# Optimization experiments

Measured on AMD Instinct MI355X. Metric: run time of the kernel, lower is better.

Reference implementation:

```python
import jax, jax.numpy as jnp
import numpy as np

B, S, D = 4, 2048, 2048
H, HD = 16, 128
ROPE_THETA = 10000.0


def rotate_half(x):
    half = x.shape[-1] // 2
    return jnp.concatenate([-x[..., half:], x[..., :half]], axis=-1)


def setup_inputs() -> dict:
    key = jax.random.key(0)
    ks = jax.random.split(key, 5)
    scale = 1.0 / np.sqrt(D)
    x = jax.random.normal(ks[0], (B, S, D), dtype=jnp.float32)
    wq = jax.random.normal(ks[1], (D, H * HD), dtype=jnp.float32) * scale
    wk = jax.random.normal(ks[2], (D, H * HD), dtype=jnp.float32) * scale
    wv = jax.random.normal(ks[3], (D, H * HD), dtype=jnp.float32) * scale
    wo = jax.random.normal(ks[4], (H * HD, D), dtype=jnp.float32) * scale
    # RoPE frequencies: freqs_cis real/imag parts, shape [S, HD//2]
    inv_freq = 1.0 / (ROPE_THETA ** (np.arange(0, HD, 2, dtype=np.float32) / HD))
    t = np.arange(S, dtype=np.float32)
    freqs = np.outer(t, inv_freq)  # [S, HD//2]
    cos = jnp.asarray(np.cos(freqs), dtype=jnp.float32)
    sin = jnp.asarray(np.sin(freqs), dtype=jnp.float32)
    return {"x": x, "wq": wq, "wk": wk, "wv": wv, "wo": wo, "cos": cos, "sin": sin}


def reference(x, wq, wk, wv, wo, cos, sin):
    batch, seq_len, _ = x.shape
    # QKV projections (no bias), reshape to [b, h, s, d]
    q = (x @ wq).reshape(batch, seq_len, H, HD).transpose(0, 2, 1, 3)
    k = (x @ wk).reshape(batch, seq_len, H, HD).transpose(0, 2, 1, 3)
    v = (x @ wv).reshape(batch, seq_len, H, HD)  # [b, s, h, d]
    # RoPE (half-split / rotate_half convention)
    cos_full = jnp.concatenate([cos, cos], axis=-1)[None, None, :seq_len, :]
    sin_full = jnp.concatenate([sin, sin], axis=-1)[None, None, :seq_len, :]
    q = q * cos_full + rotate_half(q) * sin_full
    k = k * cos_full + rotate_half(k) * sin_full
    # Scaled dot-product attention with causal mask
    logits = jnp.einsum('bhqd,bhkd->bhqk', q, k) / jnp.sqrt(jnp.float32(HD))
    causal = jnp.tril(jnp.ones((seq_len, seq_len), dtype=bool))
    logits = jnp.where(causal[None, None, :, :], logits, -1e10)
    weights = jax.nn.softmax(logits, axis=-1)
    out = jnp.einsum('bhqk,bkhd->bqhd', weights, v)
    out = out.reshape(batch, seq_len, H * HD)
    return out @ wo
```

## Files before the change

### kernel.cpp

```cpp
#include <hip/hip_runtime.h>
#include <cstdint>
#include <cstddef>

typedef unsigned short u16;
using bf16x8  = __attribute__((ext_vector_type(8))) short;
using floatx4 = __attribute__((ext_vector_type(4))) float;

__device__ __forceinline__ u16 f2bf(float f) {
    union { float f; unsigned u; } v; v.f = f;
    unsigned r = v.u + 0x7fffu + ((v.u >> 16) & 1u);
    return (u16)(r >> 16);
}
__device__ __forceinline__ float bf2f(u16 h) {
    union { unsigned u; float f; } v; v.u = ((unsigned)h) << 16; return v.f;
}
__device__ __forceinline__ floatx4 mfma16(bf16x8 a, bf16x8 b, floatx4 c) {
    return __builtin_amdgcn_mfma_f32_16x16x32_bf16(a, b, c, 0, 0, 0);
}
using gptr_t = const __attribute__((address_space(1))) unsigned int*;
using lptr_t = __attribute__((address_space(3))) unsigned int*;
__device__ __forceinline__ void lds16(const void* g, void* l) {
    __builtin_amdgcn_global_load_lds((gptr_t)g, (lptr_t)l, 16, 0, 0);
}
typedef __attribute__((address_space(3))) const u16* lds_cp;
__device__ __forceinline__ bf16x8 dsr128(const u16* p) {
    bf16x8 r;
    asm volatile("ds_read_b128 %0, %1" : "=v"(r) : "v"((lds_cp)p));
    return r;
}

#define ATT_SCALE 0.1275758218522532f

__global__ __launch_bounds__(256) void cvt_x(const float* __restrict__ x, u16* __restrict__ xb) {
    size_t i = ((size_t)blockIdx.x * 256 + threadIdx.x) * 4;
    float4 v = *(const float4*)&x[i];
    ushort4 r; r.x = f2bf(v.x); r.y = f2bf(v.y); r.z = f2bf(v.z); r.w = f2bf(v.w);
    *(ushort4*)&xb[i] = r;
}

__global__ __launch_bounds__(256) void transpose_wall(const float* __restrict__ wq, const float* __restrict__ wk,
                                                      const float* __restrict__ wv, const float* __restrict__ wo,
                                                      u16* __restrict__ wqkvb, u16* __restrict__ wob) {
    __shared__ float t[64][65];
    const int z = blockIdx.z;
    const float* in = (z == 0) ? wq : (z == 1) ? wk : (z == 2) ? wv : wo;
    u16* out = (z < 3) ? (wqkvb + (size_t)z * 2048 * 2048) : wob;
    int k0 = blockIdx.x * 64, n0 = blockIdx.y * 64;
    int tx = threadIdx.x, ty = threadIdx.y;
#pragma unroll
    for (int i = 0; i < 16; ++i) {
        int r = i * 4 + ty;
        t[r][tx] = in[(size_t)(k0 + r) * 2048 + n0 + tx];
    }
    __syncthreads();
#pragma unroll
    for (int i = 0; i < 16; ++i) {
        int r = i * 4 + ty;
        out[(size_t)(n0 + r) * 2048 + k0 + tx] = f2bf(t[tx][r]);
    }
}

template <int MODE>
__global__ __launch_bounds__(512, 2) void gemm_bt(const u16* __restrict__ A, const u16* __restrict__ B,
                                                  u16* __restrict__ Qo, u16* __restrict__ Ko, u16* __restrict__ Vt,
                                                  float* __restrict__ Co) {
    __shared__ __align__(16) u16 sA[2][16384];
    __shared__ __align__(16) u16 sB[2][16384];

    const int nbx = (MODE == 0) ? 24 : 8;
    const int bid = blockIdx.x;
    const int q8 = (int)gridDim.x >> 3;
    const int wg = (bid & 7) * q8 + (bid >> 3);
    const int bx = wg % nbx, by = wg / nbx;
    const int m0 = by << 8, n0 = bx << 8;

    const int tid = threadIdx.x;
    const int w = tid >> 6, lane = tid & 63;
    const int wm = w >> 2, wn = w & 3;
    const int m16 = lane & 15, q4 = lane >> 4;
    const int lr = lane >> 3;
    const int lc8 = (lane & 7) ^ lr;

    const u16* Ag = A + (size_t)(m0 + w * 16 + lr) * 2048 + lc8 * 8;
    const u16* Bg = B + (size_t)(n0 + w * 16 + lr) * 2048 + lc8 * 8;

    const int swz0 = ((q4 ^ (m16 & 7)) << 3);
    const int swz1 = (((4 + q4) ^ (m16 & 7)) << 3);

    floatx4 acc[8][4];
#pragma unroll
    for (int r = 0; r < 8; ++r)
#pragma unroll
        for (int c = 0; c < 4; ++c) acc[r][c] = (floatx4)0.0f;
    bf16x8 af[4][2];
    bf16x8 bf[4][2];

#define STAGE_A(b, h, t) do { \
    lds16(Ag + (size_t)((h) * 128) * 2048 + (t) * 64,     &sA[b][(h) * 8192 + w * 1024]);       \
    lds16(Ag + (size_t)((h) * 128 + 8) * 2048 + (t) * 64, &sA[b][(h) * 8192 + w * 1024 + 512]); \
} while (0)
#define STAGE_B(b, h, t) do { \
    lds16(Bg + (size_t)((h) * 128) * 2048 + (t) * 64,     &sB[b][(h) * 8192 + w * 1024]);       \
    lds16(Bg + (size_t)((h) * 128 + 8) * 2048 + (t) * 64, &sB[b][(h) * 8192 + w * 1024 + 512]); \
} while (0)
#define BAR() __builtin_amdgcn_s_barrier()
#define WAITL0() do { asm volatile("s_waitcnt lgkmcnt(0)" ::: "memory"); __builtin_amdgcn_sched_barrier(0); } while (0)
#define WAITL8() asm volatile("s_waitcnt lgkmcnt(8)" ::: "memory")
#define LDA_(cur, mq) do { _Pragma("unroll") for (int fr = 0; fr < 4; ++fr) { \
    const u16* p = &sA[cur][(wm * 128 + (mq) * 64 + fr * 16 + m16) * 64];      \
    af[fr][0] = dsr128(&p[swz0]);                                              \
    af[fr][1] = dsr128(&p[swz1]); } } while (0)
#define LDB_(cur, nq) do { _Pragma("unroll") for (int c = 0; c < 2; ++c) {     \
    const u16* p = &sB[cur][(wn * 64 + ((nq) * 2 + c) * 16 + m16) * 64];       \
    bf[(nq) * 2 + c][0] = dsr128(&p[swz0]);                                    \
    bf[(nq) * 2 + c][1] = dsr128(&p[swz1]); } } while (0)
#define MM_(mq, nq) do { _Pragma("unroll") for (int kk = 0; kk < 2; ++kk)      \
    _Pragma("unroll") for (int fr = 0; fr < 4; ++fr)                           \
    _Pragma("unroll") for (int c = 0; c < 2; ++c)                              \
        acc[(mq) * 4 + fr][(nq) * 2 + c] =                                     \
            mfma16(af[fr][kk], bf[(nq) * 2 + c][kk], acc[(mq) * 4 + fr][(nq) * 2 + c]); } while (0)

    const int NT = 32;

    STAGE_B(0, 0, 0); STAGE_B(0, 1, 0);
    STAGE_A(0, 0, 0); STAGE_A(0, 1, 0);
    STAGE_B(1, 0, 1); STAGE_B(1, 1, 1);
    asm volatile("s_waitcnt vmcnt(4)" ::: "memory");
    __builtin_amdgcn_s_barrier();

#pragma unroll 2
    for (int t = 0; t < NT; ++t) {
        const int cur = t & 1;
        LDB_(cur, 0);
        LDA_(cur, 0);
        if (t + 1 < NT) STAGE_A(cur ^ 1, 0, t + 1);
        WAITL8();
        BAR();
        WAITL0();
        __builtin_amdgcn_s_setprio(1); MM_(0, 0); __builtin_amdgcn_s_setprio(0);
        BAR();
        LDB_(cur, 1);
        if (t + 1 < NT) STAGE_A(cur ^ 1, 1, t + 1);
        BAR();
        WAITL0();
        __builtin_amdgcn_s_setprio(1); MM_(0, 1); __builtin_amdgcn_s_setprio(0);
        BAR();
        LDA_(cur, 1);
        if (t + 2 < NT) STAGE_B(cur, 0, t + 2);
        BAR();
        WAITL0();
        __builtin_amdgcn_s_setprio(1); MM_(1, 1); __builtin_amdgcn_s_setprio(0);
        BAR();
        if (t + 2 < NT) STAGE_B(cur, 1, t + 2);
        BAR();
        __builtin_amdgcn_s_setprio(1); MM_(1, 0); __builtin_amdgcn_s_setprio(0);
        if (t + 2 < NT)      { asm volatile("s_waitcnt vmcnt(4)" ::: "memory"); }
        else if (t + 1 < NT) { asm volatile("s_waitcnt vmcnt(0)" ::: "memory"); }
        BAR();
    }

#undef STAGE_A
#undef STAGE_B
#undef BAR
#undef WAITL0
#undef WAITL8
#undef LDA_
#undef LDB_
#undef MM_

    if (MODE == 0) {
        const int which = n0 >> 11;
        if (which < 2) {
            u16* dst = (which == 0) ? Qo : Ko;
#pragma unroll
            for (int fr = 0; fr < 8; ++fr) {
                const int mb = m0 + wm * 128 + fr * 16 + q4 * 4;
#pragma unroll
                for (int c = 0; c < 4; ++c) {
                    const int n = n0 + wn * 64 + c * 16 + m16;
                    const int h = (n >> 7) & 15, d = n & 127;
#pragma unroll
                    for (int i = 0; i < 4; ++i) {
                        const int mm = mb + i;
                        const int b = mm >> 11, s = mm & 2047;
                        dst[((size_t)((b * 16 + h) * 2048 + s) << 7) + d] = f2bf(acc[fr][c][i]);
                    }
                }
            }
        } else {
#pragma unroll
            for (int fr = 0; fr < 8; ++fr) {
                const int mb = m0 + wm * 128 + fr * 16 + q4 * 4;
                const int b = mb >> 11, s = mb & 2047;
#pragma unroll
                for (int c = 0; c < 4; ++c) {
                    const int n = n0 + wn * 64 + c * 16 + m16;
                    const int h = (n >> 7) & 15, d = n & 127;
                    ushort4 pk;
                    pk.x = f2bf(acc[fr][c][0]); pk.y = f2bf(acc[fr][c][1]);
                    pk.z = f2bf(acc[fr][c][2]); pk.w = f2bf(acc[fr][c][3]);
                    *(ushort4*)&Vt[((size_t)((b * 16 + h) * 128 + d)) * 2048 + s] = pk;
                }
            }
        }
    } else {
#pragma unroll
        for (int fr = 0; fr < 8; ++fr) {
            const int mb = m0 + wm * 128 + fr * 16 + q4 * 4;
#pragma unroll
            for (int c = 0; c < 4; ++c) {
                const int n = n0 + wn * 64 + c * 16 + m16;
#pragma unroll
                for (int i = 0; i < 4; ++i)
                    Co[(size_t)(mb + i) * 2048 + n] = acc[fr][c][i];
            }
        }
    }
}

__global__ __launch_bounds__(256) void rope_qk(u16* __restrict__ Q, u16* __restrict__ K,
                                               const float* __restrict__ cosb, const float* __restrict__ sinb) {
    int t = blockIdx.x * 256 + threadIdx.x;
    int d4 = (t & 15) * 4;
    int row = t >> 4;
    int s = row & 2047;
    float4 cs = *(const float4*)&cosb[s * 64 + d4];
    float4 sn = *(const float4*)&sinb[s * 64 + d4];
    size_t base = (size_t)row * 128;
    ushort4 qlo = *(ushort4*)&Q[base + d4];
    ushort4 qhi = *(ushort4*)&Q[base + 64 + d4];
    ushort4 klo = *(ushort4*)&K[base + d4];
    ushort4 khi = *(ushort4*)&K[base + 64 + d4];
    float ql[4] = {bf2f(qlo.x), bf2f(qlo.y), bf2f(qlo.z), bf2f(qlo.w)};
    float qh[4] = {bf2f(qhi.x), bf2f(qhi.y), bf2f(qhi.z), bf2f(qhi.w)};
    float kl[4] = {bf2f(klo.x), bf2f(klo.y), bf2f(klo.z), bf2f(klo.w)};
    float kh[4] = {bf2f(khi.x), bf2f(khi.y), bf2f(khi.z), bf2f(khi.w)};
    float c[4] = {cs.x, cs.y, cs.z, cs.w};
    float n[4] = {sn.x, sn.y, sn.z, sn.w};
    ushort4 o0, o1, o2, o3;
    u16* p0 = &o0.x; u16* p1 = &o1.x; u16* p2 = &o2.x; u16* p3 = &o3.x;
#pragma unroll
    for (int i = 0; i < 4; ++i) {
        p0[i] = f2bf((ql[i] * c[i] - qh[i] * n[i]) * ATT_SCALE);
        p1[i] = f2bf((qh[i] * c[i] + ql[i] * n[i]) * ATT_SCALE);
        p2[i] = f2bf(kl[i] * c[i] - kh[i] * n[i]);
        p3[i] = f2bf(kh[i] * c[i] + kl[i] * n[i]);
    }
    *(ushort4*)&Q[base + d4]      = o0;
    *(ushort4*)&Q[base + 64 + d4] = o1;
    *(ushort4*)&K[base + d4]      = o2;
    *(ushort4*)&K[base + 64 + d4] = o3;
}

__global__ __launch_bounds__(512) void attn_kernel(const u16* __restrict__ Q, const u16* __restrict__ K,
                                                   const u16* __restrict__ VT, u16* __restrict__ AO) {
    __shared__ __align__(16) u16 ks[64 * 136];
    __shared__ __align__(16) u16 vts[128 * 72];
    __shared__ __align__(16) u16 ps[256 * 72];
    static const int iqmap[8] = {7, 6, 5, 4, 0, 1, 2, 3};
    const int bx = blockIdx.x;
    const int iq = iqmap[bx >> 6];
    const int bh = bx & 63;
    const int b = bh >> 4, h = bh & 15;
    const u16* Qg = Q  + (size_t)bh * (2048 * 128);
    const u16* Kg = K  + (size_t)bh * (2048 * 128);
    const u16* Vg = VT + (size_t)bh * (128 * 2048);
    const int tid = threadIdx.x, w = tid >> 6, lane = tid & 63;
    const int m16 = lane & 15, q4 = lane >> 4;
    const int jn = 4 * iq + 4;

    const int qrow = iq * 256 + w * 32;
    bf16x8 qf[2][4];
#pragma unroll
    for (int rm = 0; rm < 2; ++rm)
#pragma unroll
        for (int kk = 0; kk < 4; ++kk)
            qf[rm][kk] = *(const bf16x8*)&Qg[(size_t)(qrow + rm * 16 + m16) * 128 + kk * 32 + q4 * 8];

    floatx4 o[2][8];
#pragma unroll
    for (int rm = 0; rm < 2; ++rm)
#pragma unroll
        for (int c = 0; c < 8; ++c) o[rm][c] = (floatx4)0.0f;
    float mrow[2] = {-1e30f, -1e30f}, lrow[2] = {0.0f, 0.0f};

    for (int j = 0; j < jn; ++j) {
        __syncthreads();
#pragma unroll
        for (int u = 0; u < 2; ++u) {
            int id = u * 512 + tid;
            int kr = id >> 4, kc = id & 15;
            uint4 kv = *(const uint4*)&Kg[(size_t)(j * 64 + kr) * 128 + kc * 8];
            int vr = id >> 3, vc = id & 7;
            uint4 vv = *(const uint4*)&Vg[(size_t)vr * 2048 + j * 64 + vc * 8];
            *(uint4*)&ks[kr * 136 + kc * 8] = kv;
            *(uint4*)&vts[vr * 72 + vc * 8] = vv;
        }
        __syncthreads();

        floatx4 sacc[2][4];
#pragma unroll
        for (int rm = 0; rm < 2; ++rm)
#pragma unroll
            for (int r = 0; r < 4; ++r) sacc[rm][r] = (floatx4)0.0f;
#pragma unroll
        for (int kk = 0; kk < 4; ++kk) {
            bf16x8 kb[4];
#pragma unroll
            for (int r = 0; r < 4; ++r)
                kb[r] = *(const bf16x8*)&ks[(r * 16 + m16) * 136 + kk * 32 + q4 * 8];
#pragma unroll
            for (int rm = 0; rm < 2; ++rm)
#pragma unroll
                for (int r = 0; r < 4; ++r)
                    sacc[rm][r] = mfma16(kb[r], qf[rm][kk], sacc[rm][r]);
        }

        if (j >= 4 * iq) {
#pragma unroll
            for (int rm = 0; rm < 2; ++rm) {
                const int qg = qrow + rm * 16 + m16;
#pragma unroll
                for (int r = 0; r < 4; ++r)
#pragma unroll
                    for (int i = 0; i < 4; ++i) {
                        int kg = j * 64 + r * 16 + q4 * 4 + i;
                        if (kg > qg) sacc[rm][r][i] = -1e30f;
                    }
            }
        }

#pragma unroll
        for (int rm = 0; rm < 2; ++rm) {
            float pmax = -1e30f;
#pragma unroll
            for (int r = 0; r < 4; ++r)
#pragma unroll
                for (int i = 0; i < 4; ++i) pmax = fmaxf(pmax, sacc[rm][r][i]);
            pmax = fmaxf(pmax, __shfl_xor(pmax, 16));
            pmax = fmaxf(pmax, __shfl_xor(pmax, 32));
            float mnew = fmaxf(mrow[rm], pmax);
            float alpha = __builtin_amdgcn_exp2f(mrow[rm] - mnew);
            mrow[rm] = mnew;

            float psum = 0.0f;
#pragma unroll
            for (int r = 0; r < 4; ++r) {
                float p0 = __builtin_amdgcn_exp2f(sacc[rm][r][0] - mnew);
                float p1 = __builtin_amdgcn_exp2f(sacc[rm][r][1] - mnew);
                float p2 = __builtin_amdgcn_exp2f(sacc[rm][r][2] - mnew);
                float p3 = __builtin_amdgcn_exp2f(sacc[rm][r][3] - mnew);
                psum += (p0 + p1) + (p2 + p3);
                ushort4 pk; pk.x = f2bf(p0); pk.y = f2bf(p1); pk.z = f2bf(p2); pk.w = f2bf(p3);
                *(ushort4*)&ps[(w * 32 + rm * 16 + m16) * 72 + r * 16 + q4 * 4] = pk;
            }
            psum += __shfl_xor(psum, 16);
            psum += __shfl_xor(psum, 32);
            lrow[rm] = lrow[rm] * alpha + psum;

            float abc[4];
#pragma unroll
            for (int i = 0; i < 4; ++i) abc[i] = __shfl(alpha, q4 * 4 + i);
#pragma unroll
            for (int c = 0; c < 8; ++c)
#pragma unroll
                for (int i = 0; i < 4; ++i) o[rm][c][i] *= abc[i];
        }

#pragma unroll
        for (int kk = 0; kk < 2; ++kk) {
            bf16x8 pa[2];
#pragma unroll
            for (int rm = 0; rm < 2; ++rm)
                pa[rm] = *(const bf16x8*)&ps[(w * 32 + rm * 16 + m16) * 72 + kk * 32 + q4 * 8];
#pragma unroll
            for (int ch = 0; ch < 2; ++ch) {
                bf16x8 vb[4];
#pragma unroll
                for (int c = 0; c < 4; ++c)
                    vb[c] = *(const bf16x8*)&vts[((ch * 4 + c) * 16 + m16) * 72 + kk * 32 + q4 * 8];
#pragma unroll
                for (int rm = 0; rm < 2; ++rm)
#pragma unroll
                    for (int c = 0; c < 4; ++c)
                        o[rm][ch * 4 + c] = mfma16(pa[rm], vb[c], o[rm][ch * 4 + c]);
            }
        }
    }

#pragma unroll
    for (int rm = 0; rm < 2; ++rm) {
        float linv = __builtin_amdgcn_rcpf(lrow[rm]);
        float li[4];
#pragma unroll
        for (int i = 0; i < 4; ++i) li[i] = __shfl(linv, q4 * 4 + i);
#pragma unroll
        for (int c = 0; c < 8; ++c)
#pragma unroll
            for (int i = 0; i < 4; ++i) {
                int s = qrow + rm * 16 + q4 * 4 + i;
                int d = c * 16 + m16;
                AO[((size_t)(b * 2048 + s)) * 2048 + h * 128 + d] = f2bf(o[rm][c][i] * li[i]);
            }
    }
}

extern "C" void kernel_launch(void* const* d_in, const int* in_sizes, int n_in,
                              void* d_out, int out_size, void* d_ws, size_t ws_size,
                              hipStream_t stream) {
    const float* x    = (const float*)d_in[0];
    const float* wq   = (const float*)d_in[1];
    const float* wk   = (const float*)d_in[2];
    const float* wv   = (const float*)d_in[3];
    const float* wo   = (const float*)d_in[4];
    const float* cosb = (const float*)d_in[5];
    const float* sinb = (const float*)d_in[6];
    float* out = (float*)d_out;

    char* ws = (char*)d_ws;
    u16* xb    = (u16*)(ws);
    u16* AO    = xb;
    u16* wqkvb = (u16*)(ws + 33554432);
    u16* wob   = (u16*)(ws + 58720256);
    u16* Qb    = (u16*)(ws + 67108864);
    u16* Kb    = (u16*)(ws + 100663296);
    u16* Vtb   = (u16*)(ws + 134217728);

    cvt_x<<<16384, 256, 0, stream>>>(x, xb);
    transpose_wall<<<dim3(32, 32, 4), dim3(64, 4), 0, stream>>>(wq, wk, wv, wo, wqkvb, wob);

    gemm_bt<0><<<768, 512, 0, stream>>>(xb, wqkvb, Qb, Kb, Vtb, nullptr);
    rope_qk<<<8192, 256, 0, stream>>>(Qb, Kb, cosb, sinb);
    attn_kernel<<<512, 512, 0, stream>>>(Qb, Kb, Vtb, AO);
    gemm_bt<1><<<256, 512, 0, stream>>>(AO, wob, nullptr, nullptr, nullptr, out);
}
```

Baseline: 568.9 us.

## Prefetch next K/V tile into registers and raise wave priority around MFMAs

Software-pipelines the attention kernel's K/V loads: the global loads for tile j+1 are issued into registers right after tile j is written to LDS, so their latency overlaps the QK and PV compute instead of stalling before each tile. The two __syncthreads are replaced with raw s_barrier calls plus explicit lgkmcnt waits. s_setprio is raised around the MFMA blocks to favour matrix issue. The cost is extra registers for the prefetched tile, which may lower occupancy, and the hand-placed barriers rely on correct ordering of the LDS writes.

```diff
diff --git a/kernel.cpp b/kernel.cpp
--- a/kernel.cpp
+++ b/kernel.cpp
@@ -284,25 +284,40 @@
         for (int c = 0; c < 8; ++c) o[rm][c] = (floatx4)0.0f;
     float mrow[2] = {-1e30f, -1e30f}, lrow[2] = {0.0f, 0.0f};
 
+    const int kr0 = tid >> 4,          kc0 = tid & 15;
+    const int kr1 = (512 + tid) >> 4,  kc1 = tid & 15;
+    const int vr0 = tid >> 3,          vc0 = tid & 7;
+    const int vr1 = (512 + tid) >> 3,  vc1 = tid & 7;
+    uint4 kreg0, kreg1, vreg0, vreg1;
+
+#define LOADKV(j) do { \
+    kreg0 = *(const uint4*)&Kg[(size_t)((j) * 64 + kr0) * 128 + kc0 * 8]; \
+    kreg1 = *(const uint4*)&Kg[(size_t)((j) * 64 + kr1) * 128 + kc1 * 8]; \
+    vreg0 = *(const uint4*)&Vg[(size_t)vr0 * 2048 + (j) * 64 + vc0 * 8];  \
+    vreg1 = *(const uint4*)&Vg[(size_t)vr1 * 2048 + (j) * 64 + vc1 * 8];  \
+} while (0)
+
+    LOADKV(0);
+
     for (int j = 0; j < jn; ++j) {
-        __syncthreads();
-#pragma unroll
-        for (int u = 0; u < 2; ++u) {
-            int id = u * 512 + tid;
-            int kr = id >> 4, kc = id & 15;
-            uint4 kv = *(const uint4*)&Kg[(size_t)(j * 64 + kr) * 128 + kc * 8];
-            int vr = id >> 3, vc = id & 7;
-            uint4 vv = *(const uint4*)&Vg[(size_t)vr * 2048 + j * 64 + vc * 8];
-            *(uint4*)&ks[kr * 136 + kc * 8] = kv;
-            *(uint4*)&vts[vr * 72 + vc * 8] = vv;
-        }
-        __syncthreads();
+        asm volatile("" ::: "memory");
+        __builtin_amdgcn_s_barrier();
+        asm volatile("" ::: "memory");
+        *(uint4*)&ks[kr0 * 136 + kc0 * 8] = kreg0;
+        *(uint4*)&ks[kr1 * 136 + kc1 * 8] = kreg1;
+        *(uint4*)&vts[vr0 * 72 + vc0 * 8] = vreg0;
+        *(uint4*)&vts[vr1 * 72 + vc1 * 8] = vreg1;
+        if (j + 1 < jn) LOADKV(j + 1);
+        asm volatile("s_waitcnt lgkmcnt(0)" ::: "memory");
+        __builtin_amdgcn_s_barrier();
+        asm volatile("" ::: "memory");
 
         floatx4 sacc[2][4];
 #pragma unroll
         for (int rm = 0; rm < 2; ++rm)
 #pragma unroll
             for (int r = 0; r < 4; ++r) sacc[rm][r] = (floatx4)0.0f;
+        __builtin_amdgcn_s_setprio(1);
 #pragma unroll
         for (int kk = 0; kk < 4; ++kk) {
             bf16x8 kb[4];
@@ -315,6 +330,7 @@
                 for (int r = 0; r < 4; ++r)
                     sacc[rm][r] = mfma16(kb[r], qf[rm][kk], sacc[rm][r]);
         }
+        __builtin_amdgcn_s_setprio(0);
 
         if (j >= 4 * iq) {
 #pragma unroll
@@ -373,6 +389,7 @@
 #pragma unroll
             for (int rm = 0; rm < 2; ++rm)
                 pa[rm] = *(const bf16x8*)&ps[(w * 32 + rm * 16 + m16) * 72 + kk * 32 + q4 * 8];
+            __builtin_amdgcn_s_setprio(1);
 #pragma unroll
             for (int ch = 0; ch < 2; ++ch) {
                 bf16x8 vb[4];
@@ -385,8 +402,10 @@
                     for (int c = 0; c < 4; ++c)
                         o[rm][ch * 4 + c] = mfma16(pa[rm], vb[c], o[rm][ch * 4 + c]);
             }
-        }
-    }
+            __builtin_amdgcn_s_setprio(0);
+        }
+    }
+#undef LOADKV
 
 #pragma unroll
     for (int rm = 0; rm < 2; ++rm) {
```

New measurement: 564.1 us. No clear change (-0.9%).
